# Kernel optimization log

Hardware: AMD Instinct MI355X
Metric: run time of the kernel (lower is better)

Reference implementation:

```python
import jax, jax.numpy as jnp
import numpy as np

EPS = 1e-5  # torch BatchNorm default


def setup_inputs() -> dict:
    key = jax.random.key(0)
    ks = jax.random.split(key, 8)
    B, Q, S, C = 4, 256, 128, 256
    feats = [2 * C, 256, 64, 1]  # opt['num_features']
    inp = {
        "support_features": jax.random.normal(ks[0], (B, S, C), dtype=jnp.float32),
        "query_features": jax.random.normal(ks[1], (B, Q, C), dtype=jnp.float32),
    }
    for i in range(3):
        fan_in, fan_out = feats[i], feats[i + 1]
        std = np.sqrt(2.0 / (fan_in + fan_out))  # xavier_normal on conv weight
        inp[f"W{i}"] = jax.random.normal(ks[2 + i], (fan_out, fan_in), dtype=jnp.float32) * std
        inp[f"b{i}"] = jnp.zeros((fan_out,), dtype=jnp.float32)
        inp[f"g{i}"] = jnp.ones((fan_out,), dtype=jnp.float32)   # BN weight
        inp[f"bt{i}"] = jnp.zeros((fan_out,), dtype=jnp.float32)  # BN bias
    return inp


def _bn_relu(x, g, bt):
    # x: [B, N, C]; BatchNorm1d training-mode stats over batch and length dims
    mean = jnp.mean(x, axis=(0, 1))
    var = jnp.mean(jnp.square(x - mean), axis=(0, 1))  # biased var, as torch BN
    return jax.nn.relu((x - mean) * (g * jax.lax.rsqrt(var + EPS)) + bt)


def reference(support_features, query_features,
              W0, b0, g0, bt0, W1, b1, g1, bt1, W2, b2, g2, bt2):
    B, S, C = support_features.shape
    Q = query_features.shape[1]
    # pairwise concat: [B, Q, S, 2C]
    uq = jnp.broadcast_to(query_features[:, :, None, :], (B, Q, S, C))
    us = jnp.broadcast_to(support_features[:, None, :, :], (B, Q, S, C))
    x = jnp.concatenate([uq, us], axis=3).reshape(B, Q * S, 2 * C)
    # 1x1 conv == matmul over channel dim
    x = _bn_relu(jnp.einsum('bnc,oc->bno', x, W0) + b0, g0, bt0)
    x = _bn_relu(jnp.einsum('bnc,oc->bno', x, W1) + b1, g1, bt1)
    x = _bn_relu(jnp.einsum('bnc,oc->bno', x, W2) + b2, g2, bt2)
    # back to [B, C_out, Q, S]
    return jnp.transpose(x, (0, 2, 1)).reshape(B, -1, Q, S)
```

## Files before the change

kernel.cpp:

```cpp
#include <hip/hip_runtime.h>
#include <hip/hip_bf16.h>


typedef __attribute__((ext_vector_type(4))) float f32x4;
typedef __attribute__((ext_vector_type(8))) short s16x8;

#define BN_EPS 1e-5f
#define INV_N  (1.0f/131072.0f)

#define LEAFA(g)   ((g)*16)
#define ROOTA      256
#define GATEA(g)   (272 + (g)*16)
#define REP_A      1024
#define LEAFB(g)   (5120 + (g)*16)
#define ROOTB      5376
#define GATEB(g)   (5392 + (g)*16)
#define CNT_ZERO   5696

__device__ __forceinline__ unsigned pk_bf16(float a, float b) {
  float2 t; t.x = a; t.y = b;
  __hip_bfloat162 h = __float22bfloat162_rn(t);
  return *reinterpret_cast<unsigned*>(&h);
}
__device__ __forceinline__ void split2(float a, float b, unsigned& uh, unsigned& ul) {
  uh = pk_bf16(a, b);
  float ha = __uint_as_float(uh << 16);
  float hb = __uint_as_float(uh & 0xFFFF0000u);
  ul = pk_bf16(a - ha, b - hb);
}

__device__ __forceinline__ unsigned a_ld(const unsigned* p) {
  return __hip_atomic_load(p, __ATOMIC_RELAXED, __HIP_MEMORY_SCOPE_AGENT);
}
__device__ __forceinline__ float a_ldf(const float* p) {
  return __hip_atomic_load(p, __ATOMIC_RELAXED, __HIP_MEMORY_SCOPE_AGENT);
}
__device__ __forceinline__ void a_st(unsigned* p, unsigned v) {
  __hip_atomic_store(p, v, __ATOMIC_RELAXED, __HIP_MEMORY_SCOPE_AGENT);
}
__device__ __forceinline__ unsigned a_add(unsigned* p) {
  return __hip_atomic_fetch_add(p, 1u, __ATOMIC_RELAXED, __HIP_MEMORY_SCOPE_AGENT);
}

union frag_u { s16x8 v; unsigned u[4]; };

struct Args {
  const float *Sf, *Qf, *W0, *b0, *g0, *bt0, *W1, *b1, *g1, *bt1, *W2, *b2, *g2, *bt2;
  float *Aq, *As, *ws0s, *ws1f, *ws2f, *out;
  unsigned *cnt;
};

__global__ __launch_bounds__(64) void k_g0(Args a)
{
  int bi = blockIdx.x, t = threadIdx.x;
  if (bi == 384) {
    for (int i = t; i < 4096; i += 64) a.ws1f[i] = 0.0f;
    if (t < 32) a.ws2f[t] = 0.0f;
    for (int i = t; i < CNT_ZERO; i += 64) a.cnt[i] = 0u;
    return;
  }
  int l15 = t & 15, quad = t >> 4;
  int chunk = bi >> 2, ntile = bi & 3;
  bool isQ = (chunk < 64);
  const float* X; float* Out; int m0, koff;
  if (isQ) { m0 = chunk * 16; X = a.Qf; Out = a.Aq; koff = 0; }
  else     { m0 = (chunk - 64) * 16; X = a.Sf; Out = a.As; koff = 256; }
  int n0 = ntile * 64;

  f32x4 acc[4] = {};
#pragma unroll
  for (int ko = 0; ko < 256; ko += 32) {
    const float* row = X + (m0 + l15) * 256 + ko + quad * 8;
    f32x4 v0 = *(const f32x4*)(row);
    f32x4 v1 = *(const f32x4*)(row + 4);
    frag_u ah, al;
#pragma unroll
    for (int j = 0; j < 2; j++) {
      split2(v0[2 * j], v0[2 * j + 1], ah.u[j], al.u[j]);
      split2(v1[2 * j], v1[2 * j + 1], ah.u[2 + j], al.u[2 + j]);
    }
#pragma unroll
    for (int nt = 0; nt < 4; nt++) {
      const float* wrow = a.W0 + (n0 + nt * 16 + l15) * 512 + koff + ko + quad * 8;
      f32x4 w0v = *(const f32x4*)(wrow);
      f32x4 w1v = *(const f32x4*)(wrow + 4);
      frag_u bh, bl;
      split2(w0v[0], w0v[1], bh.u[0], bl.u[0]);
      split2(w0v[2], w0v[3], bh.u[1], bl.u[1]);
      split2(w1v[0], w1v[1], bh.u[2], bl.u[2]);
      split2(w1v[2], w1v[3], bh.u[3], bl.u[3]);
      acc[nt] = __builtin_amdgcn_mfma_f32_16x16x32_bf16(ah.v, bh.v, acc[nt], 0, 0, 0);
      acc[nt] = __builtin_amdgcn_mfma_f32_16x16x32_bf16(al.v, bh.v, acc[nt], 0, 0, 0);
      acc[nt] = __builtin_amdgcn_mfma_f32_16x16x32_bf16(ah.v, bl.v, acc[nt], 0, 0, 0);
    }
  }
#pragma unroll
  for (int nt = 0; nt < 4; nt++) {
    int o = n0 + nt * 16 + l15;
    float bias = isQ ? 0.0f : a.b0[o];
    float cs = 0, cs2 = 0;
#pragma unroll
    for (int r = 0; r < 4; r++) {
      float y = acc[nt][r] + bias;
      Out[(m0 + quad * 4 + r) * 256 + o] = y;
      cs += y; cs2 += y * y;
    }
    cs  += __shfl_xor(cs, 16);  cs  += __shfl_xor(cs, 32);
    cs2 += __shfl_xor(cs2, 16); cs2 += __shfl_xor(cs2, 32);
    if (quad == 0) {
      a.ws0s[chunk * 512 + o] = cs;
      a.ws0s[chunk * 512 + 256 + o] = cs2;
    }
  }
}

__device__ __forceinline__ void bn0_finalize(const Args& a, int t, float* sh_a0c0)
{
  int o = t;
  float sumY = 0, cross = 0, SQ2 = 0, SS2 = 0;
#pragma unroll
  for (int b = 0; b < 4; b++) {
    float sq1 = 0, sq2 = 0, ss1 = 0, ss2 = 0;
#pragma unroll
    for (int c = 0; c < 16; c++) {
      sq1 += a.ws0s[(b * 16 + c) * 512 + o];
      sq2 += a.ws0s[(b * 16 + c) * 512 + 256 + o];
    }
#pragma unroll
    for (int c = 0; c < 8; c++) {
      ss1 += a.ws0s[(64 + b * 8 + c) * 512 + o];
      ss2 += a.ws0s[(64 + b * 8 + c) * 512 + 256 + o];
    }
    SQ2 += sq2; SS2 += ss2;
    sumY += 128.0f * sq1 + 256.0f * ss1;
    cross += sq1 * ss1;
  }
  float mean = sumY * INV_N;
  float var = (128.0f * SQ2 + 256.0f * SS2 + 2.0f * cross) * INV_N - mean * mean;
  float aa = a.g0[o] * rsqrtf(var + BN_EPS);
  sh_a0c0[o] = aa;
  sh_a0c0[256 + o] = a.bt0[o] - mean * aa;
}

__global__ __launch_bounds__(256, 2) void k_f(Args a)
{
  int bi = blockIdx.x, t = threadIdx.x;
  int w = t >> 6, l = t & 63, l15 = l & 15, quad = l >> 4;
  __shared__ ushort w1f[2048 * 8];
  __shared__ float sh_a0c0[512];
  __shared__ float red[2][4][4][16];
  __shared__ float sh_tot[128];
  __shared__ float sh_a1c1[128];
  __shared__ float rs[16], rs2[16];
  __shared__ float sh_fin[2];
  __shared__ int s_finA;

#pragma unroll
  for (int i = 0; i < 8; i++) {
    int fr = i * 256 + t;
    int kk = fr >> 8, r = fr & 255, nt = r >> 6, ln = r & 63;
    const float* src = a.W1 + (nt * 16 + (ln & 15)) * 256 + kk * 32 + (ln >> 4) * 8;
    f32x4 v0 = *(const f32x4*)(src);
    f32x4 v1 = *(const f32x4*)(src + 4);
    frag_u z;
    z.u[0] = pk_bf16(v0[0], v0[1]); z.u[1] = pk_bf16(v0[2], v0[3]);
    z.u[2] = pk_bf16(v1[0], v1[1]); z.u[3] = pk_bf16(v1[2], v1[3]);
    *(s16x8*)(w1f + fr * 8) = z.v;
  }
  bn0_finalize(a, t, sh_a0c0);
  __syncthreads();

  int b_ = bi >> 7, rem = bi & 127, qt = rem >> 3, st = rem & 7;
  const float* asrow = a.As + ((b_ << 7) + st * 16 + l15) * 256;
  const float* aqrow[4];
#pragma unroll
  for (int mt = 0; mt < 4; mt++)
    aqrow[mt] = a.Aq + ((b_ << 8) + qt * 16 + w * 4 + mt) * 256;

  f32x4 acc[4][4] = {};
#pragma unroll
  for (int kk = 0; kk < 8; kk++) {
    int obase = kk * 32 + quad * 8;
    f32x4 a0v0 = *(const f32x4*)(sh_a0c0 + obase);
    f32x4 a0v1 = *(const f32x4*)(sh_a0c0 + obase + 4);
    f32x4 c0v0 = *(const f32x4*)(sh_a0c0 + 256 + obase);
    f32x4 c0v1 = *(const f32x4*)(sh_a0c0 + 256 + obase + 4);
    f32x4 as0 = *(const f32x4*)(asrow + obase);
    f32x4 as1 = *(const f32x4*)(asrow + obase + 4);

    s16x8 zh[4];
#pragma unroll
    for (int mt = 0; mt < 4; mt++) {
      f32x4 aq0 = *(const f32x4*)(aqrow[mt] + obase);
      f32x4 aq1 = *(const f32x4*)(aqrow[mt] + obase + 4);
      f32x4 z0 = (aq0 + as0) * a0v0 + c0v0;
      f32x4 z1 = (aq1 + as1) * a0v1 + c0v1;
      frag_u zz;
      zz.u[0] = pk_bf16(fmaxf(z0[0], 0.0f), fmaxf(z0[1], 0.0f));
      zz.u[1] = pk_bf16(fmaxf(z0[2], 0.0f), fmaxf(z0[3], 0.0f));
      zz.u[2] = pk_bf16(fmaxf(z1[0], 0.0f), fmaxf(z1[1], 0.0f));
      zz.u[3] = pk_bf16(fmaxf(z1[2], 0.0f), fmaxf(z1[3], 0.0f));
      zh[mt] = zz.v;
    }
#pragma unroll
    for (int nt = 0; nt < 4; nt++) {
      s16x8 bw = *(const s16x8*)(w1f + ((kk * 4 + nt) * 64 + l) * 8);
#pragma unroll
      for (int mt = 0; mt < 4; mt++)
        acc[mt][nt] = __builtin_amdgcn_mfma_f32_16x16x32_bf16(zh[mt], bw, acc[mt][nt], 0, 0, 0);
    }
  }

  float biasv[4];
#pragma unroll
  for (int nt = 0; nt < 4; nt++) biasv[nt] = a.b1[nt * 16 + l15];
  unsigned ku01[4][4], ku23[4][4];
  float s[4] = {0, 0, 0, 0}, s2[4] = {0, 0, 0, 0};
#pragma unroll
  for (int mt = 0; mt < 4; mt++) {
#pragma unroll
    for (int nt = 0; nt < 4; nt++) {
      float y0 = acc[mt][nt][0] + biasv[nt];
      float y1 = acc[mt][nt][1] + biasv[nt];
      float y2v = acc[mt][nt][2] + biasv[nt];
      float y3 = acc[mt][nt][3] + biasv[nt];
      unsigned u01 = pk_bf16(y0, y1), u23 = pk_bf16(y2v, y3);
      ku01[mt][nt] = u01; ku23[mt][nt] = u23;
      float f0 = __uint_as_float(u01 << 16), f1 = __uint_as_float(u01 & 0xFFFF0000u);
      float f2 = __uint_as_float(u23 << 16), f3 = __uint_as_float(u23 & 0xFFFF0000u);
      s[nt]  += f0 + f1 + f2 + f3;
      s2[nt] += f0 * f0 + f1 * f1 + f2 * f2 + f3 * f3;
    }
  }
#pragma unroll
  for (int nt = 0; nt < 4; nt++) {
    float v = s[nt], v2 = s2[nt];
    v  += __shfl_xor(v, 16);  v  += __shfl_xor(v, 32);
    v2 += __shfl_xor(v2, 16); v2 += __shfl_xor(v2, 32);
    if (quad == 0) { red[0][w][nt][l15] = v; red[1][w][nt][l15] = v2; }
  }
  __syncthreads();
  if (t < 128) {
    int which = t >> 6, j = t & 63, nt = j >> 4, jl = j & 15;
    float v = red[which][0][nt][jl] + red[which][1][nt][jl] +
              red[which][2][nt][jl] + red[which][3][nt][jl];
    atomicAdd(&a.ws1f[(bi & 31) * 128 + t], v);
  }

  asm volatile("s_waitcnt vmcnt(0)" ::: "memory");
  __syncthreads();
  if (t == 0) {
    int g = bi & 15;
    unsigned old = a_add(&a.cnt[LEAFA(g)]);
    int fin = 0;
    if (old == 31u) {
      unsigned r = a_add(&a.cnt[ROOTA]);
      fin = (r == 15u);
    }
    s_finA = fin;
  }
  __syncthreads();
  if (s_finA) {
    if (t < 128) {
      float accv = 0;
#pragma unroll
      for (int c = 0; c < 32; c++)
        accv += a_ldf(&a.ws1f[c * 128 + t]);
      sh_tot[t] = accv;
    }
    __syncthreads();
    if (t < 64) {
      float mean = sh_tot[t] * INV_N;
      float var = sh_tot[64 + t] * INV_N - mean * mean;
      float aa = a.g1[t] * rsqrtf(var + BN_EPS);
      sh_a1c1[t] = aa;
      sh_a1c1[64 + t] = a.bt1[t] - mean * aa;
    }
    __syncthreads();
    if (t < 128) {
      unsigned uv = __float_as_uint(sh_a1c1[t]);
#pragma unroll
      for (int r = 0; r < 32; r++)
        a_st(&a.cnt[REP_A + r * 128 + t], uv);
    }
    asm volatile("s_waitcnt vmcnt(0)" ::: "memory");
    __syncthreads();
    if (t == 0) {
#pragma unroll
      for (int i = 0; i < 16; i++) a_st(&a.cnt[GATEA(i)], 1u);
    }
  }
  if (t == 0) {
    int g = bi & 15;
    while (a_ld(&a.cnt[GATEA(g)]) == 0u) __builtin_amdgcn_s_sleep(32);
  }
  __syncthreads();
  if (t < 128)
    sh_a1c1[t] = __uint_as_float(a_ld(&a.cnt[REP_A + (bi & 31) * 128 + t]));
  __syncthreads();

  float a1v[4], c1v[4], w2v[4];
#pragma unroll
  for (int nt = 0; nt < 4; nt++) {
    int j = nt * 16 + l15;
    a1v[nt] = sh_a1c1[j]; c1v[nt] = sh_a1c1[64 + j]; w2v[nt] = a.W2[j];
  }
  float b2v = a.b2[0];
  float y2k[4][4];
  float ls = 0, ls2 = 0;
#pragma unroll
  for (int mt = 0; mt < 4; mt++) {
    float part[4] = {0, 0, 0, 0};
#pragma unroll
    for (int nt = 0; nt < 4; nt++) {
      unsigned u01 = ku01[mt][nt], u23 = ku23[mt][nt];
      float f0 = __uint_as_float(u01 << 16), f1 = __uint_as_float(u01 & 0xFFFF0000u);
      float f2 = __uint_as_float(u23 << 16), f3 = __uint_as_float(u23 & 0xFFFF0000u);
      part[0] += fmaxf(a1v[nt] * f0 + c1v[nt], 0.0f) * w2v[nt];
      part[1] += fmaxf(a1v[nt] * f1 + c1v[nt], 0.0f) * w2v[nt];
      part[2] += fmaxf(a1v[nt] * f2 + c1v[nt], 0.0f) * w2v[nt];
      part[3] += fmaxf(a1v[nt] * f3 + c1v[nt], 0.0f) * w2v[nt];
    }
#pragma unroll
    for (int r = 0; r < 4; r++) {
      float pv = part[r];
      pv += __shfl_xor(pv, 1); pv += __shfl_xor(pv, 2);
      pv += __shfl_xor(pv, 4); pv += __shfl_xor(pv, 8);
      float y = pv + b2v;
      y2k[mt][r] = y;
      if (l15 == 0) { ls += y; ls2 += y * y; }
    }
  }
  if (l15 == 0) { rs[t >> 4] = ls; rs2[t >> 4] = ls2; }
  __syncthreads();
  if (t == 0) {
    float sv = 0, sv2 = 0;
#pragma unroll
    for (int i = 0; i < 16; i++) { sv += rs[i]; sv2 += rs2[i]; }
    atomicAdd(&a.ws2f[(bi & 15) * 2], sv);
    atomicAdd(&a.ws2f[(bi & 15) * 2 + 1], sv2);
  }

  asm volatile("s_waitcnt vmcnt(0)" ::: "memory");
  __syncthreads();
  if (t == 0) {
    int g = bi & 15;
    unsigned old = a_add(&a.cnt[LEAFB(g)]);
    if (old == 31u) {
      unsigned r = a_add(&a.cnt[ROOTB]);
      if (r == 15u) {
        float sv = 0, sv2 = 0;
#pragma unroll
        for (int c = 0; c < 16; c++) {
          sv  += a_ldf(&a.ws2f[c * 2]);
          sv2 += a_ldf(&a.ws2f[c * 2 + 1]);
        }
        float mean = sv * INV_N;
        float var = sv2 * INV_N - mean * mean;
        float aa = a.g2[0] * rsqrtf(var + BN_EPS);
        float cc = a.bt2[0] - mean * aa;
        unsigned ua = __float_as_uint(aa), uc = __float_as_uint(cc);
#pragma unroll
        for (int i = 0; i < 16; i++) {
          a_st(&a.cnt[GATEB(i) + 1], ua);
          a_st(&a.cnt[GATEB(i) + 2], uc);
        }
        asm volatile("s_waitcnt vmcnt(0)" ::: "memory");
#pragma unroll
        for (int i = 0; i < 16; i++) a_st(&a.cnt[GATEB(i)], 1u);
      }
    }
    int gg = bi & 15;
    while (a_ld(&a.cnt[GATEB(gg)]) == 0u) __builtin_amdgcn_s_sleep(32);
    sh_fin[0] = __uint_as_float(a_ld(&a.cnt[GATEB(gg) + 1]));
    sh_fin[1] = __uint_as_float(a_ld(&a.cnt[GATEB(gg) + 2]));
  }
  __syncthreads();
  float aav = sh_fin[0], ccv = sh_fin[1];

#pragma unroll
  for (int mt = 0; mt < 4; mt++) {
    if (l15 == 0) {
      int q = qt * 16 + w * 4 + mt;
      int P = ((b_ * 256 + q) * 128) + st * 16 + quad * 4;
      f32x4 o;
#pragma unroll
      for (int r = 0; r < 4; r++) o[r] = fmaxf(aav * y2k[mt][r] + ccv, 0.0f);
      *(f32x4*)(a.out + P) = o;
    }
  }
}

extern "C" void kernel_launch(void* const* d_in, const int* in_sizes, int n_in,
                              void* d_out, int out_size, void* d_ws, size_t ws_size,
                              hipStream_t stream)
{
  float* ws = (float*)d_ws;
  Args a;
  a.Sf  = (const float*)d_in[0];
  a.Qf  = (const float*)d_in[1];
  a.W0  = (const float*)d_in[2];
  a.b0  = (const float*)d_in[3];
  a.g0  = (const float*)d_in[4];
  a.bt0 = (const float*)d_in[5];
  a.W1  = (const float*)d_in[6];
  a.b1  = (const float*)d_in[7];
  a.g1  = (const float*)d_in[8];
  a.bt1 = (const float*)d_in[9];
  a.W2  = (const float*)d_in[10];
  a.b2  = (const float*)d_in[11];
  a.g2  = (const float*)d_in[12];
  a.bt2 = (const float*)d_in[13];

  a.Aq   = ws;
  a.As   = ws + 262144;
  a.ws0s = ws + 524288;
  a.ws1f = ws + 573440;
  a.ws2f = ws + 577536;
  a.cnt  = (unsigned*)(ws + 577568);
  a.out  = (float*)d_out;

  k_g0<<<385, 64, 0, stream>>>(a);
  k_f <<<512, 256, 0, stream>>>(a);
}
```

Baseline: 126.9 us.

## Replace float atomics with per-block partials and two-level tree reduction

Each block now stores its BN1 and BN2 partial sums to its own slot instead of doing atomicAdd into 32- or 16-way shared slots. A two-level tree (32 leaf groups of 16 blocks, then a root) gathers the partials, and the result is broadcast to 32 gates. Zeroing the float accumulators in the first kernel is no longer needed. This removes contention on the atomic adds, at the cost of serial gather loads in the leaf and root finisher blocks and a larger workspace.

```diff
diff --git a/kernel.cpp b/kernel.cpp
--- a/kernel.cpp
+++ b/kernel.cpp
@@ -9,13 +9,12 @@
 #define INV_N  (1.0f/131072.0f)
 
 #define LEAFA(g)   ((g)*16)
-#define ROOTA      256
-#define GATEA(g)   (272 + (g)*16)
-#define REP_A      1024
-#define LEAFB(g)   (5120 + (g)*16)
-#define ROOTB      5376
-#define GATEB(g)   (5392 + (g)*16)
-#define CNT_ZERO   5696
+#define ROOTA      512
+#define GATEA(g)   (528 + (g)*16)
+#define LEAFB(g)   (1040 + (g)*16)
+#define ROOTB      1552
+#define GATEB(g)   (1568 + (g)*16)
+#define CNT_ZERO   2080
 
 __device__ __forceinline__ unsigned pk_bf16(float a, float b) {
   float2 t; t.x = a; t.y = b;
@@ -38,6 +37,9 @@
 __device__ __forceinline__ void a_st(unsigned* p, unsigned v) {
   __hip_atomic_store(p, v, __ATOMIC_RELAXED, __HIP_MEMORY_SCOPE_AGENT);
 }
+__device__ __forceinline__ void a_stf(float* p, float v) {
+  __hip_atomic_store(p, v, __ATOMIC_RELAXED, __HIP_MEMORY_SCOPE_AGENT);
+}
 __device__ __forceinline__ unsigned a_add(unsigned* p) {
   return __hip_atomic_fetch_add(p, 1u, __ATOMIC_RELAXED, __HIP_MEMORY_SCOPE_AGENT);
 }
@@ -46,7 +48,7 @@
 
 struct Args {
   const float *Sf, *Qf, *W0, *b0, *g0, *bt0, *W1, *b1, *g1, *bt1, *W2, *b2, *g2, *bt2;
-  float *Aq, *As, *ws0s, *ws1f, *ws2f, *out;
+  float *Aq, *As, *ws0s, *ws1p, *ws1g, *ws1r, *ws2p, *ws2g, *out;
   unsigned *cnt;
 };
 
@@ -54,8 +56,6 @@
 {
   int bi = blockIdx.x, t = threadIdx.x;
   if (bi == 384) {
-    for (int i = t; i < 4096; i += 64) a.ws1f[i] = 0.0f;
-    if (t < 32) a.ws2f[t] = 0.0f;
     for (int i = t; i < CNT_ZERO; i += 64) a.cnt[i] = 0u;
     return;
   }
@@ -153,7 +153,7 @@
   __shared__ float sh_a1c1[128];
   __shared__ float rs[16], rs2[16];
   __shared__ float sh_fin[2];
-  __shared__ int s_finA;
+  __shared__ int s_role;
 
 #pragma unroll
   for (int i = 0; i < 8; i++) {
@@ -244,59 +244,69 @@
     int which = t >> 6, j = t & 63, nt = j >> 4, jl = j & 15;
     float v = red[which][0][nt][jl] + red[which][1][nt][jl] +
               red[which][2][nt][jl] + red[which][3][nt][jl];
-    atomicAdd(&a.ws1f[(bi & 31) * 128 + t], v);
+    a_stf(&a.ws1p[bi * 128 + t], v);
   }
 
   asm volatile("s_waitcnt vmcnt(0)" ::: "memory");
   __syncthreads();
+  int g = bi & 31;
   if (t == 0) {
-    int g = bi & 15;
     unsigned old = a_add(&a.cnt[LEAFA(g)]);
-    int fin = 0;
-    if (old == 31u) {
-      unsigned r = a_add(&a.cnt[ROOTA]);
-      fin = (r == 15u);
-    }
-    s_finA = fin;
-  }
-  __syncthreads();
-  if (s_finA) {
+    s_role = (old == 15u) ? 1 : 0;
+  }
+  __syncthreads();
+  if (s_role) {
     if (t < 128) {
-      float accv = 0;
-#pragma unroll
-      for (int c = 0; c < 32; c++)
-        accv += a_ldf(&a.ws1f[c * 128 + t]);
-      sh_tot[t] = accv;
-    }
-    __syncthreads();
-    if (t < 64) {
-      float mean = sh_tot[t] * INV_N;
-      float var = sh_tot[64 + t] * INV_N - mean * mean;
-      float aa = a.g1[t] * rsqrtf(var + BN_EPS);
-      sh_a1c1[t] = aa;
-      sh_a1c1[64 + t] = a.bt1[t] - mean * aa;
-    }
-    __syncthreads();
-    if (t < 128) {
-      unsigned uv = __float_as_uint(sh_a1c1[t]);
-#pragma unroll
-      for (int r = 0; r < 32; r++)
-        a_st(&a.cnt[REP_A + r * 128 + t], uv);
+      float sum = 0;
+#pragma unroll
+      for (int c = 0; c < 16; c++)
+        sum += a_ldf(&a.ws1p[(g + c * 32) * 128 + t]);
+      a_stf(&a.ws1g[g * 128 + t], sum);
     }
     asm volatile("s_waitcnt vmcnt(0)" ::: "memory");
     __syncthreads();
     if (t == 0) {
-#pragma unroll
-      for (int i = 0; i < 16; i++) a_st(&a.cnt[GATEA(i)], 1u);
+      unsigned r = a_add(&a.cnt[ROOTA]);
+      s_role = (r == 31u) ? 2 : 1;
+    }
+    __syncthreads();
+    if (s_role == 2) {
+      if (t < 128) {
+        float tot = 0;
+#pragma unroll
+        for (int gg = 0; gg < 32; gg++)
+          tot += a_ldf(&a.ws1g[gg * 128 + t]);
+        sh_tot[t] = tot;
+      }
+      __syncthreads();
+      if (t < 64) {
+        float mean = sh_tot[t] * INV_N;
+        float var = sh_tot[64 + t] * INV_N - mean * mean;
+        float aa = a.g1[t] * rsqrtf(var + BN_EPS);
+        sh_a1c1[t] = aa;
+        sh_a1c1[64 + t] = a.bt1[t] - mean * aa;
+      }
+      __syncthreads();
+      if (t < 128) {
+        float uv = sh_a1c1[t];
+#pragma unroll
+        for (int r2 = 0; r2 < 32; r2++)
+          a_stf(&a.ws1r[r2 * 128 + t], uv);
+      }
+      asm volatile("s_waitcnt vmcnt(0)" ::: "memory");
+      __syncthreads();
+      if (t == 0) {
+#pragma unroll
+        for (int i = 0; i < 32; i++) a_st(&a.cnt[GATEA(i)], 1u);
+      }
     }
   }
   if (t == 0) {
-    int g = bi & 15;
     while (a_ld(&a.cnt[GATEA(g)]) == 0u) __builtin_amdgcn_s_sleep(32);
   }
   __syncthreads();
   if (t < 128)
-    sh_a1c1[t] = __uint_as_float(a_ld(&a.cnt[REP_A + (bi & 31) * 128 + t]));
+    sh_a1c1[t] = a_ldf(&a.ws1r[g * 128 + t]);
   __syncthreads();
 
   float a1v[4], c1v[4], w2v[4];
@@ -337,23 +347,32 @@
     float sv = 0, sv2 = 0;
 #pragma unroll
     for (int i = 0; i < 16; i++) { sv += rs[i]; sv2 += rs2[i]; }
-    atomicAdd(&a.ws2f[(bi & 15) * 2], sv);
-    atomicAdd(&a.ws2f[(bi & 15) * 2 + 1], sv2);
+    a_stf(&a.ws2p[bi * 2], sv);
+    a_stf(&a.ws2p[bi * 2 + 1], sv2);
   }
 
   asm volatile("s_waitcnt vmcnt(0)" ::: "memory");
   __syncthreads();
   if (t == 0) {
-    int g = bi & 15;
     unsigned old = a_add(&a.cnt[LEAFB(g)]);
-    if (old == 31u) {
+    if (old == 15u) {
+      float s0 = 0, s1 = 0;
+#pragma unroll
+      for (int c = 0; c < 16; c++) {
+        int m = g + c * 32;
+        s0 += a_ldf(&a.ws2p[m * 2]);
+        s1 += a_ldf(&a.ws2p[m * 2 + 1]);
+      }
+      a_stf(&a.ws2g[g * 2], s0);
+      a_stf(&a.ws2g[g * 2 + 1], s1);
+      asm volatile("s_waitcnt vmcnt(0)" ::: "memory");
       unsigned r = a_add(&a.cnt[ROOTB]);
-      if (r == 15u) {
+      if (r == 31u) {
         float sv = 0, sv2 = 0;
 #pragma unroll
-        for (int c = 0; c < 16; c++) {
-          sv  += a_ldf(&a.ws2f[c * 2]);
-          sv2 += a_ldf(&a.ws2f[c * 2 + 1]);
+        for (int gg = 0; gg < 32; gg++) {
+          sv  += a_ldf(&a.ws2g[gg * 2]);
+          sv2 += a_ldf(&a.ws2g[gg * 2 + 1]);
         }
         float mean = sv * INV_N;
         float var = sv2 * INV_N - mean * mean;
@@ -361,19 +380,18 @@
         float cc = a.bt2[0] - mean * aa;
         unsigned ua = __float_as_uint(aa), uc = __float_as_uint(cc);
 #pragma unroll
-        for (int i = 0; i < 16; i++) {
+        for (int i = 0; i < 32; i++) {
           a_st(&a.cnt[GATEB(i) + 1], ua);
           a_st(&a.cnt[GATEB(i) + 2], uc);
         }
         asm volatile("s_waitcnt vmcnt(0)" ::: "memory");
 #pragma unroll
-        for (int i = 0; i < 16; i++) a_st(&a.cnt[GATEB(i)], 1u);
-      }
-    }
-    int gg = bi & 15;
-    while (a_ld(&a.cnt[GATEB(gg)]) == 0u) __builtin_amdgcn_s_sleep(32);
-    sh_fin[0] = __uint_as_float(a_ld(&a.cnt[GATEB(gg) + 1]));
-    sh_fin[1] = __uint_as_float(a_ld(&a.cnt[GATEB(gg) + 2]));
+        for (int i = 0; i < 32; i++) a_st(&a.cnt[GATEB(i)], 1u);
+      }
+    }
+    while (a_ld(&a.cnt[GATEB(g)]) == 0u) __builtin_amdgcn_s_sleep(32);
+    sh_fin[0] = __uint_as_float(a_ld(&a.cnt[GATEB(g) + 1]));
+    sh_fin[1] = __uint_as_float(a_ld(&a.cnt[GATEB(g) + 2]));
   }
   __syncthreads();
   float aav = sh_fin[0], ccv = sh_fin[1];
@@ -415,9 +433,12 @@
   a.Aq   = ws;
   a.As   = ws + 262144;
   a.ws0s = ws + 524288;
-  a.ws1f = ws + 573440;
-  a.ws2f = ws + 577536;
-  a.cnt  = (unsigned*)(ws + 577568);
+  a.ws1p = ws + 573440;
+  a.ws1g = ws + 638976;
+  a.ws1r = ws + 643072;
+  a.ws2p = ws + 647168;
+  a.ws2g = ws + 648192;
+  a.cnt  = (unsigned*)(ws + 648256);
   a.out  = (float*)d_out;
 
   k_g0<<<385, 64, 0, stream>>>(a);
```

New measurement: 125.7 us. About the same (-1.0%).
